# Kernel tuning notes

Measured on AMD Instinct MI355X. Metric: run time of the kernel, lower is better.

The kernel has to match this reference:

```python
import jax, jax.numpy as jnp
import numpy as np

N, H, DDE, NH = 256, 256, 64, 4

def setup_inputs() -> dict:
    key = jax.random.key(0)
    ks = jax.random.split(key, 12)
    rn = lambda k, s, sc=1.0: (jax.random.normal(k, s) * sc).astype(jnp.float32)
    return {
        "action_hidden_state": rn(ks[0], (N, H)),
        "goal_hidden_state": rn(ks[1], (N, H)),
        "goal": rn(ks[2], (N, 2)),
        "action": rn(ks[3], (N, 2)),
        "W_dist": rn(ks[4], (8, DDE), 0.3),          # distEmbedding Linear(8, dde)
        "b_dist": jnp.zeros((DDE,), jnp.float32),
        "W_gate": rn(ks[5], (DDE, H), 0.1),          # gateFC Linear(dde, H)
        "b_gate": jnp.zeros((H,), jnp.float32),
        "w": rn(ks[6], (NH, 1, H, H), 0.06),         # GAT per-head projection
        "a": rn(ks[7], (1, 1, 2 * H, 1), 0.06),      # attention vector
        "bias": jnp.zeros((H,), jnp.float32),
    }

def reference(action_hidden_state, goal_hidden_state, goal, action,
              W_dist, b_dist, W_gate, b_gate, w, a, bias):
    n = goal.shape[0]
    # --- InteractionGate.cal_gate: x1[i,j] = x[j], x2[i,j] = x[i] ---
    g1 = jnp.broadcast_to(goal[None, :, :], (n, n, 2))
    g2 = jnp.broadcast_to(goal[:, None, :], (n, n, 2))
    a1 = jnp.broadcast_to(action[None, :, :], (n, n, 2))
    a2 = jnp.broadcast_to(action[:, None, :], (n, n, 2))
    dist = jnp.concatenate([a2, g2, a1, g1], axis=-1)                 # [n,n,8]
    gate = jax.nn.sigmoid(jax.nn.relu(dist @ W_dist + b_dist) @ W_gate + b_gate)  # [n,n,H]
    # temp_action_1[i,j] = action_hidden_state[j]
    gate_action = gate * jnp.tanh(action_hidden_state[None, :, :])    # [n,n,H]
    # diagonal entries replaced by goal_hidden_state (mask_goal = eye)
    eye = jnp.eye(n, dtype=bool)[:, :, None]
    gated_h = jnp.where(eye, goal_hidden_state[None, :, :], gate_action)  # [n,n,H]

    # --- GAT assembly: h_self[i,k] = ahs[i]; h_other = cat(ahs, gated_h) ---
    h_other = jnp.concatenate([action_hidden_state[:, None, :], gated_h], axis=1)  # [n,n+1,H]

    wm = w[:, 0]          # [NH,H,H]
    a_flat = a[0, 0, :, 0]  # [2H]
    f = wm.shape[-1]
    n_head = wm.shape[0]
    # h_self rows along k are all identical -> project once per (head, node)
    hsp = jnp.einsum('nh,zhf->znf', action_hidden_state, wm)          # [NH,n,f]
    hop = jnp.einsum('nkh,zhf->znkf', h_other, wm)                    # [NH,n,n+1,f]
    # cat([h_self', h_other']) @ a  ==  h_self'@a[:f] + h_other'@a[f:]
    score = (hsp @ a_flat[:f])[:, :, None] + hop @ a_flat[f:]         # [NH,n,n+1]
    e = jnp.where(score > 0, score, 0.2 * score)                      # LeakyReLU(0.2)
    alpha = jax.nn.softmax(e, axis=-1)                                # softmax over neighbors
    # h_attn = matmul(h_other, w) == hop; weighted sum over k, mean over heads
    out = jnp.einsum('znk,znkf->nf', alpha, hop) / n_head             # [n,f]
    return jax.nn.relu(out) + bias
```

## Files before the change

kernel.cpp:

```cpp
#include <hip/hip_runtime.h>
#include <hip/hip_bf16.h>

#define NN 256
#define HH 256

typedef __attribute__((ext_vector_type(8))) short short8;
typedef __attribute__((ext_vector_type(4))) float f32x4;

__device__ __forceinline__ ushort f2bf(float x) {
    __hip_bfloat16 h = __float2bfloat16(x);
    return *reinterpret_cast<ushort*>(&h);
}
__device__ __forceinline__ float bf2f(ushort u) {
    __hip_bfloat16 h = *reinterpret_cast<__hip_bfloat16*>(&u);
    return __bfloat162float(h);
}
__device__ __forceinline__ float fast_rcp(float x) {
    return __builtin_amdgcn_rcpf(x);
}
__device__ __forceinline__ float fast_tanh(float x) {
    float e = __expf(2.0f * x);
    return 1.0f - 2.0f * fast_rcp(e + 1.0f);
}
template <int CTRL>
__device__ __forceinline__ float dpp_add(float x) {
    int y = __builtin_amdgcn_update_dpp(0, __float_as_int(x), CTRL, 0xF, 0xF, true);
    return x + __int_as_float(y);
}
template <int CTRL>
__device__ __forceinline__ float dpp_max(float x) {
    int y = __builtin_amdgcn_update_dpp(0, __float_as_int(x), CTRL, 0xF, 0xF, true);
    return fmaxf(x, __int_as_float(y));
}
__device__ __forceinline__ float red16(float v) {
    v = dpp_add<0xB1>(v); v = dpp_add<0x4E>(v);
    v = dpp_add<0x141>(v); v = dpp_add<0x140>(v);
    return v;
}
__device__ __forceinline__ float red16max(float v) {
    v = dpp_max<0xB1>(v); v = dpp_max<0x4E>(v);
    v = dpp_max<0x141>(v); v = dpp_max<0x140>(v);
    return v;
}

#define WS_P   0
#define WS_Q   16384
#define WS_T   32768
#define WS_WA  98304
#define WS_WB  99328
#define WS_WGT 100352
#define WS_PV  108544
#define WS_ML  632832
#define WS_W2H 636928
#define WS_W2L 768000

__global__ __launch_bounds__(256) void precompute_kernel(
    const float* __restrict__ ahs, const float* __restrict__ goal,
    const float* __restrict__ action, const float* __restrict__ Wd,
    const float* __restrict__ b_dist, const float* __restrict__ Wg,
    const float* __restrict__ w, const float* __restrict__ a,
    float* __restrict__ ws)
{
    const int b = blockIdx.x;
    const int t = threadIdx.x;
    const int wid  = t >> 6;
    const int lane = t & 63;
    float* P  = ws + WS_P;
    float* Q  = ws + WS_Q;
    float* T  = ws + WS_T;
    float* WA = ws + WS_WA;
    float* WB = ws + WS_WB;
    ushort* WgT  = (ushort*)(ws + WS_WGT);
    ushort* W2hi = (ushort*)(ws + WS_W2H);
    ushort* W2lo = (ushort*)(ws + WS_W2L);

    __shared__ __align__(16) float tile[64][65];

    if (b < 16) {
        const int z  = b >> 2;
        const int rg = b & 3;
        const int hbase = rg*64 + wid*16;
        const f32x4 aB = *(const f32x4*)(a + lane*4);
        const f32x4 aA = *(const f32x4*)(a + HH + lane*4);
#pragma unroll 4
        for (int rr = 0; rr < 16; ++rr) {
            const int h = hbase + rr;
            const f32x4 w4 = *(const f32x4*)(w + z*HH*HH + h*HH + lane*4);
            float dA = w4.x*aA.x + w4.y*aA.y + w4.z*aA.z + w4.w*aA.w;
            float dB = w4.x*aB.x + w4.y*aB.y + w4.z*aB.z + w4.w*aB.w;
#pragma unroll
            for (int off = 32; off; off >>= 1) {
                dA += __shfl_xor(dA, off);
                dB += __shfl_xor(dB, off);
            }
            if (lane == 0) { WA[z*HH + h] = dA; WB[z*HH + h] = dB; }
        }
    } else if (b < 80) {
        const int idx = b - 16;
        const int k0  = (idx >> 2) * 64;
        const int f0  = (idx & 3) * 64;
        const int ff  = t & 63;
#pragma unroll 4
        for (int i = 0; i < 16; ++i) {
            const int kk = i*4 + wid;
            tile[kk][ff] = w[(k0 + kk)*HH + f0 + ff];
        }
        __syncthreads();
#pragma unroll 4
        for (int i = 0; i < 16; ++i) {
            const int fl = i*4 + wid;
            float x = tile[ff][fl];
            ushort hi = f2bf(x);
            ushort lo = f2bf(x - bf2f(hi));
            W2hi[(size_t)(f0 + fl)*1024 + k0 + ff] = hi;
            W2lo[(size_t)(f0 + fl)*1024 + k0 + ff] = lo;
        }
    } else if (b < 144) {
        const int i = (b - 80)*4 + wid;
        const int d = lane;
        float a0 = action[2*i], a1 = action[2*i+1];
        float g0 = goal[2*i],   g1 = goal[2*i+1];
        P[i*64 + d] = a0*Wd[0*64+d] + a1*Wd[1*64+d]
                    + g0*Wd[2*64+d] + g1*Wd[3*64+d] + b_dist[d];
        Q[i*64 + d] = a0*Wd[4*64+d] + a1*Wd[5*64+d]
                    + g0*Wd[6*64+d] + g1*Wd[7*64+d];
    } else if (b < 208) {
        const int d = b - 144;
        WgT[t*64 + d] = f2bf(Wg[d*HH + t]);
    } else {
        const int idx = ((b - 208)*256 + t)*4;
        float4 v = *(const float4*)(ahs + idx);
        float4 o;
        o.x = fast_tanh(v.x); o.y = fast_tanh(v.y);
        o.z = fast_tanh(v.z); o.w = fast_tanh(v.w);
        *(float4*)(T + idx) = o;
    }
}

__global__ __launch_bounds__(256, 2) void gat_partial_kernel(
    const float* __restrict__ ahs, const float* __restrict__ ghs,
    const float* __restrict__ b_gate, float* __restrict__ ws)
{
    const int n    = blockIdx.x >> 1;
    const int hh   = blockIdx.x & 1;
    const int t    = threadIdx.x;
    const int wid  = t >> 6;
    const int lane = t & 63;
    const int quad = lane >> 4;
    const int l15  = lane & 15;
    const int zg   = quad;
    const int jj   = l15;
    const int n0   = wid * 64;

    const float* P  = ws + WS_P;
    const float* Q  = ws + WS_Q;
    const float* T  = ws + WS_T;
    const float* WA = ws + WS_WA;
    const float* WB = ws + WS_WB;
    const ushort* WgT = (const ushort*)(ws + WS_WGT);
    float* PV = ws + WS_PV;
    float* ML = ws + WS_ML;

    __shared__ __align__(16) float part[2][4][16][4];
    __shared__ __align__(16) float alpha_w[4][16][4];
    __shared__ __align__(16) float vred[16][260];
    __shared__ __align__(16) ushort A_l[128*64];

    int hcol[4];
#pragma unroll
    for (int nt = 0; nt < 4; ++nt) hcol[nt] = n0 + nt*16 + l15;

    short8 bfrag[4][2];
    float  wa_reg[4][4];
    float  bgv[4], gval[4];
#pragma unroll
    for (int nt = 0; nt < 4; ++nt) {
#pragma unroll
        for (int kh = 0; kh < 2; ++kh)
            bfrag[nt][kh] = *(const short8*)(WgT + hcol[nt]*64 + kh*32 + quad*8);
#pragma unroll
        for (int z = 0; z < 4; ++z) wa_reg[z][nt] = WA[z*HH + hcol[nt]];
        bgv[nt]  = b_gate[hcol[nt]];
        gval[nt] = ghs[n*HH + hcol[nt]];
    }

    {
        const int jl = t >> 1;
        const int kh = t & 1;
        const float* prow = P + n*64 + kh*32;
        const float* qrow = Q + (hh*128 + jl)*64 + kh*32;
        ushort hv[32];
#pragma unroll
        for (int c = 0; c < 8; ++c) {
            f32x4 pq = *(const f32x4*)(prow + c*4);
            f32x4 qq = *(const f32x4*)(qrow + c*4);
            hv[c*4+0] = f2bf(fmaxf(pq.x + qq.x, 0.f));
            hv[c*4+1] = f2bf(fmaxf(pq.y + qq.y, 0.f));
            hv[c*4+2] = f2bf(fmaxf(pq.z + qq.z, 0.f));
            hv[c*4+3] = f2bf(fmaxf(pq.w + qq.w, 0.f));
        }
        char* rb = (char*)A_l + jl*128;
        const int sw = (jl & 7) << 4;
#pragma unroll
        for (int c2 = 0; c2 < 4; ++c2) {
            const int off = (kh*64 + c2*16) ^ sw;
            *(short8*)(rb + off) = *(const short8*)(hv + c2*8);
        }
    }

    float vacc[4][4];
    {
        float av[4];
#pragma unroll
        for (int nt = 0; nt < 4; ++nt) av[nt] = ahs[n*HH + hcol[nt]];
#pragma unroll
        for (int z = 0; z < 4; ++z)
#pragma unroll
            for (int nt = 0; nt < 4; ++nt)
                vacc[z][nt] = (hh == 0 && quad == 0) ? av[nt] : 0.f;
    }

    float cz_r, m_r, l_r;
    {
        float pc = 0.f, ps = 0.f;
        const int hb = jj*16;
#pragma unroll
        for (int i4 = 0; i4 < 4; ++i4) {
            f32x4 av = *(const f32x4*)(ahs + n*HH + hb + i4*4);
            f32x4 wb = *(const f32x4*)(WB + zg*HH + hb + i4*4);
            f32x4 wa = *(const f32x4*)(WA + zg*HH + hb + i4*4);
            pc = fmaf(av.x, wb.x, pc); pc = fmaf(av.y, wb.y, pc);
            pc = fmaf(av.z, wb.z, pc); pc = fmaf(av.w, wb.w, pc);
            ps = fmaf(av.x, wa.x, ps); ps = fmaf(av.y, wa.y, ps);
            ps = fmaf(av.z, wa.z, ps); ps = fmaf(av.w, wa.w, ps);
        }
        pc = red16(pc); ps = red16(ps);
        cz_r = pc;
        if (hh == 0) {
            float sc = pc + ps;
            m_r = sc > 0.f ? sc : 0.2f * sc;
            l_r = 1.0f;
        } else {
            m_r = -__builtin_inff();
            l_r = 0.0f;
        }
    }

    __syncthreads();

    float tval[4][4];
    {
        const int j0 = hh*128;
#pragma unroll
        for (int r = 0; r < 4; ++r) {
            const int jg = j0 + quad*4 + r;
#pragma unroll
            for (int nt = 0; nt < 4; ++nt)
                tval[nt][r] = T[jg*HH + hcol[nt]];
        }
    }

    for (int cc = 0; cc < 8; ++cc) {
        const int j0  = hh*128 + cc*16;
        const int par = cc & 1;

        const int jl = cc*16 + l15;
        const char* rb = (const char*)A_l + jl*128;
        const int sw = (l15 & 7) << 4;
        short8 afrag0 = *(const short8*)(rb + ((quad*16) ^ sw));
        short8 afrag1 = *(const short8*)(rb + ((64 + quad*16) ^ sw));

        f32x4 acc[4];
#pragma unroll
        for (int nt = 0; nt < 4; ++nt) {
            f32x4 a4 = (f32x4){0.f,0.f,0.f,0.f};
            a4 = __builtin_amdgcn_mfma_f32_16x16x32_bf16(afrag0, bfrag[nt][0], a4, 0, 0, 0);
            a4 = __builtin_amdgcn_mfma_f32_16x16x32_bf16(afrag1, bfrag[nt][1], a4, 0, 0, 0);
            acc[nt] = a4;
        }

        float vals[4][4];
#pragma unroll
        for (int r = 0; r < 4; ++r) {
            const int jg = j0 + quad*4 + r;
            const bool diag = (jg == n);
#pragma unroll
            for (int nt = 0; nt < 4; ++nt) {
                float u = acc[nt][r] + bgv[nt];
                float g = fast_rcp(1.0f + __expf(-u));
                vals[nt][r] = diag ? gval[nt] : g * tval[nt][r];
            }
        }

#pragma unroll
        for (int z = 0; z < 4; ++z) {
            float pp[4];
#pragma unroll
            for (int r = 0; r < 4; ++r) {
                float s = 0.f;
#pragma unroll
                for (int nt = 0; nt < 4; ++nt)
                    s = fmaf(vals[nt][r], wa_reg[z][nt], s);
                pp[r] = red16(s);
            }
            if (l15 == z) {
#pragma unroll
                for (int r = 0; r < 4; ++r)
                    part[par][z][quad*4 + r][wid] = pp[r];
            }
        }
        __syncthreads();

        float tnext[4][4];
        if (cc < 7) {
            const int j1 = j0 + 16;
#pragma unroll
            for (int r = 0; r < 4; ++r) {
                const int jg = j1 + quad*4 + r;
#pragma unroll
                for (int nt = 0; nt < 4; ++nt)
                    tnext[nt][r] = T[jg*HH + hcol[nt]];
            }
        }

        float scl0, scl1, scl2, scl3;
        {
            f32x4 pr = *(const f32x4*)&part[par][zg][jj][0];
            float s = cz_r + ((pr.x + pr.y) + (pr.z + pr.w));
            float e = s > 0.f ? s : 0.2f * s;
            float mx = red16max(e);
            float m_new = fmaxf(m_r, mx);
            float at = __expf(e - m_new);
            float ss = red16(at);
            float scale = __expf(m_r - m_new);
            l_r = l_r * scale + ss;
            m_r = m_new;
            alpha_w[wid][jj][zg] = at;
            scl0 = __shfl(scale, 0);
            scl1 = __shfl(scale, 16);
            scl2 = __shfl(scale, 32);
            scl3 = __shfl(scale, 48);
        }
#pragma unroll
        for (int nt = 0; nt < 4; ++nt) {
            vacc[0][nt] *= scl0; vacc[1][nt] *= scl1;
            vacc[2][nt] *= scl2; vacc[3][nt] *= scl3;
        }
#pragma unroll
        for (int r = 0; r < 4; ++r) {
            f32x4 al = *(const f32x4*)&alpha_w[wid][quad*4 + r][0];
#pragma unroll
            for (int nt = 0; nt < 4; ++nt) {
                float v = vals[nt][r];
                vacc[0][nt] = fmaf(al.x, v, vacc[0][nt]);
                vacc[1][nt] = fmaf(al.y, v, vacc[1][nt]);
                vacc[2][nt] = fmaf(al.z, v, vacc[2][nt]);
                vacc[3][nt] = fmaf(al.w, v, vacc[3][nt]);
            }
        }
        if (cc < 7) {
#pragma unroll
            for (int nt = 0; nt < 4; ++nt)
#pragma unroll
                for (int r = 0; r < 4; ++r)
                    tval[nt][r] = tnext[nt][r];
        }
    }

#pragma unroll
    for (int z = 0; z < 4; ++z)
#pragma unroll
        for (int nt = 0; nt < 4; ++nt)
            vred[quad*4 + z][hcol[nt]] = vacc[z][nt];
    __syncthreads();
#pragma unroll
    for (int z = 0; z < 4; ++z) {
        float s = (vred[0*4+z][t] + vred[1*4+z][t]) + (vred[2*4+z][t] + vred[3*4+z][t]);
        PV[((size_t)(hh*4 + z)*NN + n)*HH + t] = s;
    }
    if (wid == 0 && l15 == 0) {
        ML[((hh*4 + zg)*NN + n)*2 + 0] = m_r;
        ML[((hh*4 + zg)*NN + n)*2 + 1] = l_r;
    }
}

__global__ __launch_bounds__(256) void gat_out_kernel(
    const float* __restrict__ bias, const float* __restrict__ ws,
    float* __restrict__ out)
{
    const int n0 = (blockIdx.x >> 4) * 16;
    const int f0 = (blockIdx.x & 15) * 16;
    const int t    = threadIdx.x;
    const int wid  = t >> 6;
    const int lane = t & 63;
    const int quad = lane >> 4;
    const int l15  = lane & 15;

    const float* PV = ws + WS_PV;
    const float* ML = ws + WS_ML;
    const ushort* W2hi = (const ushort*)(ws + WS_W2H);
    const ushort* W2lo = (const ushort*)(ws + WS_W2L);

    __shared__ __align__(16) float redc[3][16][17];
    __shared__ __align__(16) float sq[16][4][2];

    if (t < 128) {
        const int n_i = t >> 3, z = (t >> 1) & 3, q = t & 1;
        float m = ML[((q*4 + z)*NN + n0 + n_i)*2 + 0];
        float l = ML[((q*4 + z)*NN + n0 + n_i)*2 + 1];
        float mm = fmaxf(m, __shfl_xor(m, 1));
        float s  = __expf(m - mm);
        float ls = l * s;
        ls += __shfl_xor(ls, 1);
        sq[n_i][z][q] = s * fast_rcp(ls);
    }
    __syncthreads();

    f32x4 acc = (f32x4){0.f,0.f,0.f,0.f};

    const float s0 = sq[l15][wid][0];
    const float s1 = sq[l15][wid][1];
    const float* pv0 = PV + ((size_t)(0*4 + wid)*NN + n0 + l15)*HH;
    const float* pv1 = PV + ((size_t)(1*4 + wid)*NN + n0 + l15)*HH;

    for (int ks = 0; ks < 8; ++ks) {
        const int kp = ks*32 + quad*8;
        f32x4 p0a = *(const f32x4*)(pv0 + kp);
        f32x4 p0b = *(const f32x4*)(pv0 + kp + 4);
        f32x4 p1a = *(const f32x4*)(pv1 + kp);
        f32x4 p1b = *(const f32x4*)(pv1 + kp + 4);
        float v[8];
        v[0] = s0*p0a.x + s1*p1a.x; v[1] = s0*p0a.y + s1*p1a.y;
        v[2] = s0*p0a.z + s1*p1a.z; v[3] = s0*p0a.w + s1*p1a.w;
        v[4] = s0*p0b.x + s1*p1b.x; v[5] = s0*p0b.y + s1*p1b.y;
        v[6] = s0*p0b.z + s1*p1b.z; v[7] = s0*p0b.w + s1*p1b.w;
        ushort hi[8], lo[8];
#pragma unroll
        for (int c = 0; c < 8; ++c) {
            hi[c] = f2bf(v[c]);
            lo[c] = f2bf(v[c] - bf2f(hi[c]));
        }
        short8 ah = *(short8*)hi;
        short8 al = *(short8*)lo;
        const size_t boff = (size_t)(f0 + l15)*1024 + wid*256 + kp;
        short8 bh = *(const short8*)(W2hi + boff);
        short8 bl = *(const short8*)(W2lo + boff);
        acc = __builtin_amdgcn_mfma_f32_16x16x32_bf16(ah, bh, acc, 0, 0, 0);
        acc = __builtin_amdgcn_mfma_f32_16x16x32_bf16(ah, bl, acc, 0, 0, 0);
        acc = __builtin_amdgcn_mfma_f32_16x16x32_bf16(al, bh, acc, 0, 0, 0);
    }

    if (wid > 0) {
#pragma unroll
        for (int r = 0; r < 4; ++r)
            redc[wid-1][quad*4 + r][l15] = acc[r];
    }
    __syncthreads();
    if (wid == 0) {
        const int f = f0 + l15;
        float bv = bias[f];
#pragma unroll
        for (int r = 0; r < 4; ++r) {
            const int row = quad*4 + r;
            float s = acc[r]
                    + redc[0][row][l15]
                    + redc[1][row][l15]
                    + redc[2][row][l15];
            out[(size_t)(n0 + row)*HH + f] = fmaxf(0.25f * s, 0.f) + bv;
        }
    }
}

extern "C" void kernel_launch(void* const* d_in, const int* in_sizes, int n_in,
                              void* d_out, int out_size, void* d_ws, size_t ws_size,
                              hipStream_t stream)
{
    const float* ahs    = (const float*)d_in[0];
    const float* ghs    = (const float*)d_in[1];
    const float* goal   = (const float*)d_in[2];
    const float* action = (const float*)d_in[3];
    const float* Wd     = (const float*)d_in[4];
    const float* b_dist = (const float*)d_in[5];
    const float* Wg     = (const float*)d_in[6];
    const float* b_gate = (const float*)d_in[7];
    const float* w      = (const float*)d_in[8];
    const float* a      = (const float*)d_in[9];
    const float* bias   = (const float*)d_in[10];
    float* ws   = (float*)d_ws;
    float* outp = (float*)d_out;

    precompute_kernel<<<272, 256, 0, stream>>>(ahs, goal, action, Wd, b_dist, Wg, w, a, ws);
    gat_partial_kernel<<<512, 256, 0, stream>>>(ahs, ghs, b_gate, ws);
    gat_out_kernel<<<256, 256, 0, stream>>>(bias, ws, outp);
}
```

Baseline: 114.6 us.

## Fuse three kernels into one cooperative kernel with grid-wide syncs

Merges the precompute, GAT partial and output kernels into a single cooperative launch of 512 blocks, with grid.sync between phases and a union of shared-memory layouts. The goal is to remove two kernel launch gaps and the tail drain between dependent kernels. In exchange it adds the cost of grid-wide barriers, and it requires all 512 blocks to be resident at once. It falls back to the three-kernel path if the cooperative launch fails.

```diff
diff --git a/kernel.cpp b/kernel.cpp
--- a/kernel.cpp
+++ b/kernel.cpp
@@ -1,5 +1,8 @@
 #include <hip/hip_runtime.h>
 #include <hip/hip_bf16.h>
+#include <hip/hip_cooperative_groups.h>
+
+namespace cg = cooperative_groups;
 
 #define NN 256
 #define HH 256
@@ -53,6 +56,421 @@
 #define WS_ML  632832
 #define WS_W2H 636928
 #define WS_W2L 768000
+
+__global__ __launch_bounds__(256, 2) void fused_kernel(
+    const float* __restrict__ ahs, const float* __restrict__ ghs,
+    const float* __restrict__ goal, const float* __restrict__ action,
+    const float* __restrict__ Wd, const float* __restrict__ b_dist,
+    const float* __restrict__ Wg, const float* __restrict__ b_gate,
+    const float* __restrict__ w, const float* __restrict__ a,
+    const float* __restrict__ bias,
+    float* __restrict__ ws, float* __restrict__ out)
+{
+    cg::grid_group gridg = cg::this_grid();
+
+    __shared__ __align__(16) union {
+        struct { float tile[64][65]; } pa;
+        struct {
+            float part[2][4][16][4];
+            float alpha_w[4][16][4];
+            float vred[16][260];
+            ushort A_l[128*64];
+        } pb;
+        struct { float redc[3][16][17]; float sq[16][4][2]; } pc;
+    } sm;
+
+    float* P  = ws + WS_P;
+    float* Q  = ws + WS_Q;
+    float* T  = ws + WS_T;
+    float* WA = ws + WS_WA;
+    float* WB = ws + WS_WB;
+    ushort* WgT  = (ushort*)(ws + WS_WGT);
+    ushort* W2hi = (ushort*)(ws + WS_W2H);
+    ushort* W2lo = (ushort*)(ws + WS_W2L);
+    float* PV = ws + WS_PV;
+    float* ML = ws + WS_ML;
+
+    {
+        const int b = blockIdx.x;
+        const int t = threadIdx.x;
+        const int wid  = t >> 6;
+        const int lane = t & 63;
+
+        if (b < 16) {
+            const int z  = b >> 2;
+            const int rg = b & 3;
+            const int hbase = rg*64 + wid*16;
+            const f32x4 aB = *(const f32x4*)(a + lane*4);
+            const f32x4 aA = *(const f32x4*)(a + HH + lane*4);
+#pragma unroll 4
+            for (int rr = 0; rr < 16; ++rr) {
+                const int h = hbase + rr;
+                const f32x4 w4 = *(const f32x4*)(w + z*HH*HH + h*HH + lane*4);
+                float dA = w4.x*aA.x + w4.y*aA.y + w4.z*aA.z + w4.w*aA.w;
+                float dB = w4.x*aB.x + w4.y*aB.y + w4.z*aB.z + w4.w*aB.w;
+#pragma unroll
+                for (int off = 32; off; off >>= 1) {
+                    dA += __shfl_xor(dA, off);
+                    dB += __shfl_xor(dB, off);
+                }
+                if (lane == 0) { WA[z*HH + h] = dA; WB[z*HH + h] = dB; }
+            }
+        } else if (b < 80) {
+            const int idx = b - 16;
+            const int k0  = (idx >> 2) * 64;
+            const int f0  = (idx & 3) * 64;
+            const int ff  = t & 63;
+#pragma unroll 4
+            for (int i = 0; i < 16; ++i) {
+                const int kk = i*4 + wid;
+                sm.pa.tile[kk][ff] = w[(k0 + kk)*HH + f0 + ff];
+            }
+            __syncthreads();
+#pragma unroll 4
+            for (int i = 0; i < 16; ++i) {
+                const int fl = i*4 + wid;
+                float x = sm.pa.tile[ff][fl];
+                ushort hi = f2bf(x);
+                ushort lo = f2bf(x - bf2f(hi));
+                W2hi[(size_t)(f0 + fl)*1024 + k0 + ff] = hi;
+                W2lo[(size_t)(f0 + fl)*1024 + k0 + ff] = lo;
+            }
+        } else if (b < 144) {
+            const int i = (b - 80)*4 + wid;
+            const int d = lane;
+            float a0 = action[2*i], a1 = action[2*i+1];
+            float g0 = goal[2*i],   g1 = goal[2*i+1];
+            P[i*64 + d] = a0*Wd[0*64+d] + a1*Wd[1*64+d]
+                        + g0*Wd[2*64+d] + g1*Wd[3*64+d] + b_dist[d];
+            Q[i*64 + d] = a0*Wd[4*64+d] + a1*Wd[5*64+d]
+                        + g0*Wd[6*64+d] + g1*Wd[7*64+d];
+        } else if (b < 208) {
+            const int d = b - 144;
+            WgT[t*64 + d] = f2bf(Wg[d*HH + t]);
+        } else if (b < 272) {
+            const int idx = ((b - 208)*256 + t)*4;
+            float4 v = *(const float4*)(ahs + idx);
+            float4 o;
+            o.x = fast_tanh(v.x); o.y = fast_tanh(v.y);
+            o.z = fast_tanh(v.z); o.w = fast_tanh(v.w);
+            *(float4*)(T + idx) = o;
+        }
+    }
+
+    __threadfence();
+    gridg.sync();
+
+    {
+        const int n    = blockIdx.x >> 1;
+        const int hh   = blockIdx.x & 1;
+        const int t    = threadIdx.x;
+        const int wid  = t >> 6;
+        const int lane = t & 63;
+        const int quad = lane >> 4;
+        const int l15  = lane & 15;
+        const int zg   = quad;
+        const int jj   = l15;
+        const int n0   = wid * 64;
+
+        int hcol[4];
+#pragma unroll
+        for (int nt = 0; nt < 4; ++nt) hcol[nt] = n0 + nt*16 + l15;
+
+        short8 bfrag[4][2];
+        float  wa_reg[4][4];
+        float  bgv[4], gval[4];
+#pragma unroll
+        for (int nt = 0; nt < 4; ++nt) {
+#pragma unroll
+            for (int kh = 0; kh < 2; ++kh)
+                bfrag[nt][kh] = *(const short8*)(WgT + hcol[nt]*64 + kh*32 + quad*8);
+#pragma unroll
+            for (int z = 0; z < 4; ++z) wa_reg[z][nt] = WA[z*HH + hcol[nt]];
+            bgv[nt]  = b_gate[hcol[nt]];
+            gval[nt] = ghs[n*HH + hcol[nt]];
+        }
+
+        {
+            const int jl = t >> 1;
+            const int kh = t & 1;
+            const float* prow = P + n*64 + kh*32;
+            const float* qrow = Q + (hh*128 + jl)*64 + kh*32;
+            ushort hv[32];
+#pragma unroll
+            for (int c = 0; c < 8; ++c) {
+                f32x4 pq = *(const f32x4*)(prow + c*4);
+                f32x4 qq = *(const f32x4*)(qrow + c*4);
+                hv[c*4+0] = f2bf(fmaxf(pq.x + qq.x, 0.f));
+                hv[c*4+1] = f2bf(fmaxf(pq.y + qq.y, 0.f));
+                hv[c*4+2] = f2bf(fmaxf(pq.z + qq.z, 0.f));
+                hv[c*4+3] = f2bf(fmaxf(pq.w + qq.w, 0.f));
+            }
+            char* rb = (char*)sm.pb.A_l + jl*128;
+            const int sw = (jl & 7) << 4;
+#pragma unroll
+            for (int c2 = 0; c2 < 4; ++c2) {
+                const int off = (kh*64 + c2*16) ^ sw;
+                *(short8*)(rb + off) = *(const short8*)(hv + c2*8);
+            }
+        }
+
+        float vacc[4][4];
+        {
+            float av[4];
+#pragma unroll
+            for (int nt = 0; nt < 4; ++nt) av[nt] = ahs[n*HH + hcol[nt]];
+#pragma unroll
+            for (int z = 0; z < 4; ++z)
+#pragma unroll
+                for (int nt = 0; nt < 4; ++nt)
+                    vacc[z][nt] = (hh == 0 && quad == 0) ? av[nt] : 0.f;
+        }
+
+        float cz_r, m_r, l_r;
+        {
+            float pc = 0.f, ps = 0.f;
+            const int hb = jj*16;
+#pragma unroll
+            for (int i4 = 0; i4 < 4; ++i4) {
+                f32x4 av = *(const f32x4*)(ahs + n*HH + hb + i4*4);
+                f32x4 wb = *(const f32x4*)(WB + zg*HH + hb + i4*4);
+                f32x4 wa = *(const f32x4*)(WA + zg*HH + hb + i4*4);
+                pc = fmaf(av.x, wb.x, pc); pc = fmaf(av.y, wb.y, pc);
+                pc = fmaf(av.z, wb.z, pc); pc = fmaf(av.w, wb.w, pc);
+                ps = fmaf(av.x, wa.x, ps); ps = fmaf(av.y, wa.y, ps);
+                ps = fmaf(av.z, wa.z, ps); ps = fmaf(av.w, wa.w, ps);
+            }
+            pc = red16(pc); ps = red16(ps);
+            cz_r = pc;
+            if (hh == 0) {
+                float sc = pc + ps;
+                m_r = sc > 0.f ? sc : 0.2f * sc;
+                l_r = 1.0f;
+            } else {
+                m_r = -__builtin_inff();
+                l_r = 0.0f;
+            }
+        }
+
+        __syncthreads();
+
+        float tval[4][4];
+        {
+            const int j0 = hh*128;
+#pragma unroll
+            for (int r = 0; r < 4; ++r) {
+                const int jg = j0 + quad*4 + r;
+#pragma unroll
+                for (int nt = 0; nt < 4; ++nt)
+                    tval[nt][r] = T[jg*HH + hcol[nt]];
+            }
+        }
+
+        for (int cc = 0; cc < 8; ++cc) {
+            const int j0  = hh*128 + cc*16;
+            const int par = cc & 1;
+
+            const int jl = cc*16 + l15;
+            const char* rb = (const char*)sm.pb.A_l + jl*128;
+            const int sw = (l15 & 7) << 4;
+            short8 afrag0 = *(const short8*)(rb + ((quad*16) ^ sw));
+            short8 afrag1 = *(const short8*)(rb + ((64 + quad*16) ^ sw));
+
+            f32x4 acc[4];
+#pragma unroll
+            for (int nt = 0; nt < 4; ++nt) {
+                f32x4 a4 = (f32x4){0.f,0.f,0.f,0.f};
+                a4 = __builtin_amdgcn_mfma_f32_16x16x32_bf16(afrag0, bfrag[nt][0], a4, 0, 0, 0);
+                a4 = __builtin_amdgcn_mfma_f32_16x16x32_bf16(afrag1, bfrag[nt][1], a4, 0, 0, 0);
+                acc[nt] = a4;
+            }
+
+            float vals[4][4];
+#pragma unroll
+            for (int r = 0; r < 4; ++r) {
+                const int jg = j0 + quad*4 + r;
+                const bool diag = (jg == n);
+#pragma unroll
+                for (int nt = 0; nt < 4; ++nt) {
+                    float u = acc[nt][r] + bgv[nt];
+                    float g = fast_rcp(1.0f + __expf(-u));
+                    vals[nt][r] = diag ? gval[nt] : g * tval[nt][r];
+                }
+            }
+
+#pragma unroll
+            for (int z = 0; z < 4; ++z) {
+                float pp[4];
+#pragma unroll
+                for (int r = 0; r < 4; ++r) {
+                    float s = 0.f;
+#pragma unroll
+                    for (int nt = 0; nt < 4; ++nt)
+                        s = fmaf(vals[nt][r], wa_reg[z][nt], s);
+                    pp[r] = red16(s);
+                }
+                if (l15 == z) {
+#pragma unroll
+                    for (int r = 0; r < 4; ++r)
+                        sm.pb.part[par][z][quad*4 + r][wid] = pp[r];
+                }
+            }
+            __syncthreads();
+
+            float tnext[4][4];
+            if (cc < 7) {
+                const int j1 = j0 + 16;
+#pragma unroll
+                for (int r = 0; r < 4; ++r) {
+                    const int jg = j1 + quad*4 + r;
+#pragma unroll
+                    for (int nt = 0; nt < 4; ++nt)
+                        tnext[nt][r] = T[jg*HH + hcol[nt]];
+                }
+            }
+
+            float scl0, scl1, scl2, scl3;
+            {
+                f32x4 pr = *(const f32x4*)&sm.pb.part[par][zg][jj][0];
+                float s = cz_r + ((pr.x + pr.y) + (pr.z + pr.w));
+                float e = s > 0.f ? s : 0.2f * s;
+                float mx = red16max(e);
+                float m_new = fmaxf(m_r, mx);
+                float at = __expf(e - m_new);
+                float ss = red16(at);
+                float scale = __expf(m_r - m_new);
+                l_r = l_r * scale + ss;
+                m_r = m_new;
+                sm.pb.alpha_w[wid][jj][zg] = at;
+                scl0 = __shfl(scale, 0);
+                scl1 = __shfl(scale, 16);
+                scl2 = __shfl(scale, 32);
+                scl3 = __shfl(scale, 48);
+            }
+#pragma unroll
+            for (int nt = 0; nt < 4; ++nt) {
+                vacc[0][nt] *= scl0; vacc[1][nt] *= scl1;
+                vacc[2][nt] *= scl2; vacc[3][nt] *= scl3;
+            }
+#pragma unroll
+            for (int r = 0; r < 4; ++r) {
+                f32x4 al = *(const f32x4*)&sm.pb.alpha_w[wid][quad*4 + r][0];
+#pragma unroll
+                for (int nt = 0; nt < 4; ++nt) {
+                    float v = vals[nt][r];
+                    vacc[0][nt] = fmaf(al.x, v, vacc[0][nt]);
+                    vacc[1][nt] = fmaf(al.y, v, vacc[1][nt]);
+                    vacc[2][nt] = fmaf(al.z, v, vacc[2][nt]);
+                    vacc[3][nt] = fmaf(al.w, v, vacc[3][nt]);
+                }
+            }
+            if (cc < 7) {
+#pragma unroll
+                for (int nt = 0; nt < 4; ++nt)
+#pragma unroll
+                    for (int r = 0; r < 4; ++r)
+                        tval[nt][r] = tnext[nt][r];
+            }
+        }
+
+#pragma unroll
+        for (int z = 0; z < 4; ++z)
+#pragma unroll
+            for (int nt = 0; nt < 4; ++nt)
+                sm.pb.vred[quad*4 + z][hcol[nt]] = vacc[z][nt];
+        __syncthreads();
+#pragma unroll
+        for (int z = 0; z < 4; ++z) {
+            float s = (sm.pb.vred[0*4+z][t] + sm.pb.vred[1*4+z][t])
+                    + (sm.pb.vred[2*4+z][t] + sm.pb.vred[3*4+z][t]);
+            PV[((size_t)(hh*4 + z)*NN + n)*HH + t] = s;
+        }
+        if (wid == 0 && l15 == 0) {
+            ML[((hh*4 + zg)*NN + n)*2 + 0] = m_r;
+            ML[((hh*4 + zg)*NN + n)*2 + 1] = l_r;
+        }
+    }
+
+    __threadfence();
+    gridg.sync();
+
+    if (blockIdx.x < 256) {
+        const int b = blockIdx.x;
+        const int n0 = (b >> 4) * 16;
+        const int f0 = (b & 15) * 16;
+        const int t    = threadIdx.x;
+        const int wid  = t >> 6;
+        const int lane = t & 63;
+        const int quad = lane >> 4;
+        const int l15  = lane & 15;
+
+        if (t < 128) {
+            const int n_i = t >> 3, z = (t >> 1) & 3, q = t & 1;
+            float m = ML[((q*4 + z)*NN + n0 + n_i)*2 + 0];
+            float l = ML[((q*4 + z)*NN + n0 + n_i)*2 + 1];
+            float mm = fmaxf(m, __shfl_xor(m, 1));
+            float s  = __expf(m - mm);
+            float ls = l * s;
+            ls += __shfl_xor(ls, 1);
+            sm.pc.sq[n_i][z][q] = s * fast_rcp(ls);
+        }
+        __syncthreads();
+
+        f32x4 acc = (f32x4){0.f,0.f,0.f,0.f};
+
+        const float s0 = sm.pc.sq[l15][wid][0];
+        const float s1 = sm.pc.sq[l15][wid][1];
+        const float* pv0 = PV + ((size_t)(0*4 + wid)*NN + n0 + l15)*HH;
+        const float* pv1 = PV + ((size_t)(1*4 + wid)*NN + n0 + l15)*HH;
+
+        for (int ks = 0; ks < 8; ++ks) {
+            const int kp = ks*32 + quad*8;
+            f32x4 p0a = *(const f32x4*)(pv0 + kp);
+            f32x4 p0b = *(const f32x4*)(pv0 + kp + 4);
+            f32x4 p1a = *(const f32x4*)(pv1 + kp);
+            f32x4 p1b = *(const f32x4*)(pv1 + kp + 4);
+            float v[8];
+            v[0] = s0*p0a.x + s1*p1a.x; v[1] = s0*p0a.y + s1*p1a.y;
+            v[2] = s0*p0a.z + s1*p1a.z; v[3] = s0*p0a.w + s1*p1a.w;
+            v[4] = s0*p0b.x + s1*p1b.x; v[5] = s0*p0b.y + s1*p1b.y;
+            v[6] = s0*p0b.z + s1*p1b.z; v[7] = s0*p0b.w + s1*p1b.w;
+            ushort hi[8], lo[8];
+#pragma unroll
+            for (int c = 0; c < 8; ++c) {
+                hi[c] = f2bf(v[c]);
+                lo[c] = f2bf(v[c] - bf2f(hi[c]));
+            }
+            short8 ah = *(short8*)hi;
+            short8 al = *(short8*)lo;
+            const size_t boff = (size_t)(f0 + l15)*1024 + wid*256 + kp;
+            short8 bh = *(const short8*)(W2hi + boff);
+            short8 bl = *(const short8*)(W2lo + boff);
+            acc = __builtin_amdgcn_mfma_f32_16x16x32_bf16(ah, bh, acc, 0, 0, 0);
+            acc = __builtin_amdgcn_mfma_f32_16x16x32_bf16(ah, bl, acc, 0, 0, 0);
+            acc = __builtin_amdgcn_mfma_f32_16x16x32_bf16(al, bh, acc, 0, 0, 0);
+        }
+
+        if (wid > 0) {
+#pragma unroll
+            for (int r = 0; r < 4; ++r)
+                sm.pc.redc[wid-1][quad*4 + r][l15] = acc[r];
+        }
+        __syncthreads();
+        if (wid == 0) {
+            const int f = f0 + l15;
+            float bv = bias[f];
+#pragma unroll
+            for (int r = 0; r < 4; ++r) {
+                const int row = quad*4 + r;
+                float s = acc[r]
+                        + sm.pc.redc[0][row][l15]
+                        + sm.pc.redc[1][row][l15]
+                        + sm.pc.redc[2][row][l15];
+                out[(size_t)(n0 + row)*HH + f] = fmaxf(0.25f * s, 0.f) + bv;
+            }
+        }
+    }
+}
 
 __global__ __launch_bounds__(256) void precompute_kernel(
     const float* __restrict__ ahs, const float* __restrict__ goal,
@@ -489,7 +907,16 @@
     float* ws   = (float*)d_ws;
     float* outp = (float*)d_out;
 
-    precompute_kernel<<<272, 256, 0, stream>>>(ahs, goal, action, Wd, b_dist, Wg, w, a, ws);
-    gat_partial_kernel<<<512, 256, 0, stream>>>(ahs, ghs, b_gate, ws);
-    gat_out_kernel<<<256, 256, 0, stream>>>(bias, ws, outp);
-}
+    void* args[] = {
+        (void*)&ahs, (void*)&ghs, (void*)&goal, (void*)&action,
+        (void*)&Wd, (void*)&b_dist, (void*)&Wg, (void*)&b_gate,
+        (void*)&w, (void*)&a, (void*)&bias, (void*)&ws, (void*)&outp
+    };
+    hipError_t err = hipLaunchCooperativeKernel(
+        (void*)fused_kernel, dim3(512), dim3(256), args, 0, stream);
+    if (err != hipSuccess) {
+        precompute_kernel<<<272, 256, 0, stream>>>(ahs, goal, action, Wd, b_dist, Wg, w, a, ws);
+        gat_partial_kernel<<<512, 256, 0, stream>>>(ahs, ghs, b_gate, ws);
+        gat_out_kernel<<<256, 256, 0, stream>>>(bias, ws, outp);
+    }
+}
```

Result: slower. 333.1 us (+190.7%).

## Fuse GAT partial and output kernels using per-tile atomic counters

Applied to the files above, without the earlier changes.

Merges the partial-attention kernel and the output kernel into one launch. Each block bumps a per-16-node counter after writing its PV/ML partials. The hh==0 blocks then spin until all 32 contributing blocks of their tile have arrived, and compute the output tile for that tile. This removes one kernel launch and its boundary, and shares shared memory through a union. The spin-wait relies on all contributing blocks being co-resident or scheduled ahead, which risks stalls, and a guard counter breaks out of the spin.

```diff
diff --git a/kernel.cpp b/kernel.cpp
--- a/kernel.cpp
+++ b/kernel.cpp
@@ -53,6 +53,8 @@
 #define WS_ML  632832
 #define WS_W2H 636928
 #define WS_W2L 768000
+
+__device__ unsigned int g_cnt[16];
 
 __global__ __launch_bounds__(256) void precompute_kernel(
     const float* __restrict__ ahs, const float* __restrict__ goal,
@@ -76,6 +78,9 @@
 
     __shared__ __align__(16) float tile[64][65];
 
+    if (b == 0 && t < 16)
+        __hip_atomic_store(&g_cnt[t], 0u, __ATOMIC_RELAXED, __HIP_MEMORY_SCOPE_AGENT);
+
     if (b < 16) {
         const int z  = b >> 2;
         const int rg = b & 3;
@@ -137,9 +142,10 @@
     }
 }
 
-__global__ __launch_bounds__(256, 2) void gat_partial_kernel(
+__global__ __launch_bounds__(256, 2) void gat_partial_out_kernel(
     const float* __restrict__ ahs, const float* __restrict__ ghs,
-    const float* __restrict__ b_gate, float* __restrict__ ws)
+    const float* __restrict__ b_gate, const float* __restrict__ bias,
+    float* __restrict__ ws, float* __restrict__ out)
 {
     const int n    = blockIdx.x >> 1;
     const int hh   = blockIdx.x & 1;
@@ -161,253 +167,270 @@
     float* PV = ws + WS_PV;
     float* ML = ws + WS_ML;
 
-    __shared__ __align__(16) float part[2][4][16][4];
-    __shared__ __align__(16) float alpha_w[4][16][4];
-    __shared__ __align__(16) float vred[16][260];
-    __shared__ __align__(16) ushort A_l[128*64];
-
-    int hcol[4];
-#pragma unroll
-    for (int nt = 0; nt < 4; ++nt) hcol[nt] = n0 + nt*16 + l15;
-
-    short8 bfrag[4][2];
-    float  wa_reg[4][4];
-    float  bgv[4], gval[4];
-#pragma unroll
-    for (int nt = 0; nt < 4; ++nt) {
-#pragma unroll
-        for (int kh = 0; kh < 2; ++kh)
-            bfrag[nt][kh] = *(const short8*)(WgT + hcol[nt]*64 + kh*32 + quad*8);
-#pragma unroll
-        for (int z = 0; z < 4; ++z) wa_reg[z][nt] = WA[z*HH + hcol[nt]];
-        bgv[nt]  = b_gate[hcol[nt]];
-        gval[nt] = ghs[n*HH + hcol[nt]];
-    }
+    __shared__ __align__(16) union {
+        struct {
+            float part[2][4][16][4];
+            float alpha_w[4][16][4];
+            float vred[16][260];
+            ushort A_l[128*64];
+        } pb;
+        struct { float redc[3][16][17]; float sq[16][4][2]; } pc;
+    } sm;
 
     {
-        const int jl = t >> 1;
-        const int kh = t & 1;
-        const float* prow = P + n*64 + kh*32;
-        const float* qrow = Q + (hh*128 + jl)*64 + kh*32;
-        ushort hv[32];
-#pragma unroll
-        for (int c = 0; c < 8; ++c) {
-            f32x4 pq = *(const f32x4*)(prow + c*4);
-            f32x4 qq = *(const f32x4*)(qrow + c*4);
-            hv[c*4+0] = f2bf(fmaxf(pq.x + qq.x, 0.f));
-            hv[c*4+1] = f2bf(fmaxf(pq.y + qq.y, 0.f));
-            hv[c*4+2] = f2bf(fmaxf(pq.z + qq.z, 0.f));
-            hv[c*4+3] = f2bf(fmaxf(pq.w + qq.w, 0.f));
-        }
-        char* rb = (char*)A_l + jl*128;
-        const int sw = (jl & 7) << 4;
-#pragma unroll
-        for (int c2 = 0; c2 < 4; ++c2) {
-            const int off = (kh*64 + c2*16) ^ sw;
-            *(short8*)(rb + off) = *(const short8*)(hv + c2*8);
-        }
-    }
-
-    float vacc[4][4];
-    {
-        float av[4];
-#pragma unroll
-        for (int nt = 0; nt < 4; ++nt) av[nt] = ahs[n*HH + hcol[nt]];
+        auto& part    = sm.pb.part;
+        auto& alpha_w = sm.pb.alpha_w;
+        auto& vred    = sm.pb.vred;
+        auto& A_l     = sm.pb.A_l;
+
+        int hcol[4];
+#pragma unroll
+        for (int nt = 0; nt < 4; ++nt) hcol[nt] = n0 + nt*16 + l15;
+
+        short8 bfrag[4][2];
+        float  wa_reg[4][4];
+        float  bgv[4], gval[4];
+#pragma unroll
+        for (int nt = 0; nt < 4; ++nt) {
+#pragma unroll
+            for (int kh = 0; kh < 2; ++kh)
+                bfrag[nt][kh] = *(const short8*)(WgT + hcol[nt]*64 + kh*32 + quad*8);
+#pragma unroll
+            for (int z = 0; z < 4; ++z) wa_reg[z][nt] = WA[z*HH + hcol[nt]];
+            bgv[nt]  = b_gate[hcol[nt]];
+            gval[nt] = ghs[n*HH + hcol[nt]];
+        }
+
+        {
+            const int jl = t >> 1;
+            const int kh = t & 1;
+            const float* prow = P + n*64 + kh*32;
+            const float* qrow = Q + (hh*128 + jl)*64 + kh*32;
+            ushort hv[32];
+#pragma unroll
+            for (int c = 0; c < 8; ++c) {
+                f32x4 pq = *(const f32x4*)(prow + c*4);
+                f32x4 qq = *(const f32x4*)(qrow + c*4);
+                hv[c*4+0] = f2bf(fmaxf(pq.x + qq.x, 0.f));
+                hv[c*4+1] = f2bf(fmaxf(pq.y + qq.y, 0.f));
+                hv[c*4+2] = f2bf(fmaxf(pq.z + qq.z, 0.f));
+                hv[c*4+3] = f2bf(fmaxf(pq.w + qq.w, 0.f));
+            }
+            char* rb = (char*)A_l + jl*128;
+            const int sw = (jl & 7) << 4;
+#pragma unroll
+            for (int c2 = 0; c2 < 4; ++c2) {
+                const int off = (kh*64 + c2*16) ^ sw;
+                *(short8*)(rb + off) = *(const short8*)(hv + c2*8);
+            }
+        }
+
+        float vacc[4][4];
+        {
+            float av[4];
+#pragma unroll
+            for (int nt = 0; nt < 4; ++nt) av[nt] = ahs[n*HH + hcol[nt]];
+#pragma unroll
+            for (int z = 0; z < 4; ++z)
+#pragma unroll
+                for (int nt = 0; nt < 4; ++nt)
+                    vacc[z][nt] = (hh == 0 && quad == 0) ? av[nt] : 0.f;
+        }
+
+        float cz_r, m_r, l_r;
+        {
+            float pc = 0.f, ps = 0.f;
+            const int hb = jj*16;
+#pragma unroll
+            for (int i4 = 0; i4 < 4; ++i4) {
+                f32x4 av = *(const f32x4*)(ahs + n*HH + hb + i4*4);
+                f32x4 wb = *(const f32x4*)(WB + zg*HH + hb + i4*4);
+                f32x4 wa = *(const f32x4*)(WA + zg*HH + hb + i4*4);
+                pc = fmaf(av.x, wb.x, pc); pc = fmaf(av.y, wb.y, pc);
+                pc = fmaf(av.z, wb.z, pc); pc = fmaf(av.w, wb.w, pc);
+                ps = fmaf(av.x, wa.x, ps); ps = fmaf(av.y, wa.y, ps);
+                ps = fmaf(av.z, wa.z, ps); ps = fmaf(av.w, wa.w, ps);
+            }
+            pc = red16(pc); ps = red16(ps);
+            cz_r = pc;
+            if (hh == 0) {
+                float sc = pc + ps;
+                m_r = sc > 0.f ? sc : 0.2f * sc;
+                l_r = 1.0f;
+            } else {
+                m_r = -__builtin_inff();
+                l_r = 0.0f;
+            }
+        }
+
+        __syncthreads();
+
+        float tval[4][4];
+        {
+            const int j0 = hh*128;
+#pragma unroll
+            for (int r = 0; r < 4; ++r) {
+                const int jg = j0 + quad*4 + r;
+#pragma unroll
+                for (int nt = 0; nt < 4; ++nt)
+                    tval[nt][r] = T[jg*HH + hcol[nt]];
+            }
+        }
+
+        for (int cc = 0; cc < 8; ++cc) {
+            const int j0  = hh*128 + cc*16;
+            const int par = cc & 1;
+
+            const int jl = cc*16 + l15;
+            const char* rb = (const char*)A_l + jl*128;
+            const int sw = (l15 & 7) << 4;
+            short8 afrag0 = *(const short8*)(rb + ((quad*16) ^ sw));
+            short8 afrag1 = *(const short8*)(rb + ((64 + quad*16) ^ sw));
+
+            f32x4 acc[4];
+#pragma unroll
+            for (int nt = 0; nt < 4; ++nt) {
+                f32x4 a4 = (f32x4){0.f,0.f,0.f,0.f};
+                a4 = __builtin_amdgcn_mfma_f32_16x16x32_bf16(afrag0, bfrag[nt][0], a4, 0, 0, 0);
+                a4 = __builtin_amdgcn_mfma_f32_16x16x32_bf16(afrag1, bfrag[nt][1], a4, 0, 0, 0);
+                acc[nt] = a4;
+            }
+
+            float vals[4][4];
+#pragma unroll
+            for (int r = 0; r < 4; ++r) {
+                const int jg = j0 + quad*4 + r;
+                const bool diag = (jg == n);
+#pragma unroll
+                for (int nt = 0; nt < 4; ++nt) {
+                    float u = acc[nt][r] + bgv[nt];
+                    float g = fast_rcp(1.0f + __expf(-u));
+                    vals[nt][r] = diag ? gval[nt] : g * tval[nt][r];
+                }
+            }
+
+#pragma unroll
+            for (int z = 0; z < 4; ++z) {
+                float pp[4];
+#pragma unroll
+                for (int r = 0; r < 4; ++r) {
+                    float s = 0.f;
+#pragma unroll
+                    for (int nt = 0; nt < 4; ++nt)
+                        s = fmaf(vals[nt][r], wa_reg[z][nt], s);
+                    pp[r] = red16(s);
+                }
+                if (l15 == z) {
+#pragma unroll
+                    for (int r = 0; r < 4; ++r)
+                        part[par][z][quad*4 + r][wid] = pp[r];
+                }
+            }
+            __syncthreads();
+
+            float tnext[4][4];
+            if (cc < 7) {
+                const int j1 = j0 + 16;
+#pragma unroll
+                for (int r = 0; r < 4; ++r) {
+                    const int jg = j1 + quad*4 + r;
+#pragma unroll
+                    for (int nt = 0; nt < 4; ++nt)
+                        tnext[nt][r] = T[jg*HH + hcol[nt]];
+                }
+            }
+
+            float scl0, scl1, scl2, scl3;
+            {
+                f32x4 pr = *(const f32x4*)&part[par][zg][jj][0];
+                float s = cz_r + ((pr.x + pr.y) + (pr.z + pr.w));
+                float e = s > 0.f ? s : 0.2f * s;
+                float mx = red16max(e);
+                float m_new = fmaxf(m_r, mx);
+                float at = __expf(e - m_new);
+                float ss = red16(at);
+                float scale = __expf(m_r - m_new);
+                l_r = l_r * scale + ss;
+                m_r = m_new;
+                alpha_w[wid][jj][zg] = at;
+                scl0 = __shfl(scale, 0);
+                scl1 = __shfl(scale, 16);
+                scl2 = __shfl(scale, 32);
+                scl3 = __shfl(scale, 48);
+            }
+#pragma unroll
+            for (int nt = 0; nt < 4; ++nt) {
+                vacc[0][nt] *= scl0; vacc[1][nt] *= scl1;
+                vacc[2][nt] *= scl2; vacc[3][nt] *= scl3;
+            }
+#pragma unroll
+            for (int r = 0; r < 4; ++r) {
+                f32x4 al = *(const f32x4*)&alpha_w[wid][quad*4 + r][0];
+#pragma unroll
+                for (int nt = 0; nt < 4; ++nt) {
+                    float v = vals[nt][r];
+                    vacc[0][nt] = fmaf(al.x, v, vacc[0][nt]);
+                    vacc[1][nt] = fmaf(al.y, v, vacc[1][nt]);
+                    vacc[2][nt] = fmaf(al.z, v, vacc[2][nt]);
+                    vacc[3][nt] = fmaf(al.w, v, vacc[3][nt]);
+                }
+            }
+            if (cc < 7) {
+#pragma unroll
+                for (int nt = 0; nt < 4; ++nt)
+#pragma unroll
+                    for (int r = 0; r < 4; ++r)
+                        tval[nt][r] = tnext[nt][r];
+            }
+        }
+
 #pragma unroll
         for (int z = 0; z < 4; ++z)
 #pragma unroll
             for (int nt = 0; nt < 4; ++nt)
-                vacc[z][nt] = (hh == 0 && quad == 0) ? av[nt] : 0.f;
-    }
-
-    float cz_r, m_r, l_r;
-    {
-        float pc = 0.f, ps = 0.f;
-        const int hb = jj*16;
-#pragma unroll
-        for (int i4 = 0; i4 < 4; ++i4) {
-            f32x4 av = *(const f32x4*)(ahs + n*HH + hb + i4*4);
-            f32x4 wb = *(const f32x4*)(WB + zg*HH + hb + i4*4);
-            f32x4 wa = *(const f32x4*)(WA + zg*HH + hb + i4*4);
-            pc = fmaf(av.x, wb.x, pc); pc = fmaf(av.y, wb.y, pc);
-            pc = fmaf(av.z, wb.z, pc); pc = fmaf(av.w, wb.w, pc);
-            ps = fmaf(av.x, wa.x, ps); ps = fmaf(av.y, wa.y, ps);
-            ps = fmaf(av.z, wa.z, ps); ps = fmaf(av.w, wa.w, ps);
-        }
-        pc = red16(pc); ps = red16(ps);
-        cz_r = pc;
-        if (hh == 0) {
-            float sc = pc + ps;
-            m_r = sc > 0.f ? sc : 0.2f * sc;
-            l_r = 1.0f;
-        } else {
-            m_r = -__builtin_inff();
-            l_r = 0.0f;
-        }
-    }
-
+                vred[quad*4 + z][hcol[nt]] = vacc[z][nt];
+        __syncthreads();
+#pragma unroll
+        for (int z = 0; z < 4; ++z) {
+            float s = (vred[0*4+z][t] + vred[1*4+z][t]) + (vred[2*4+z][t] + vred[3*4+z][t]);
+            PV[((size_t)(hh*4 + z)*NN + n)*HH + t] = s;
+        }
+        if (wid == 0 && l15 == 0) {
+            ML[((hh*4 + zg)*NN + n)*2 + 0] = m_r;
+            ML[((hh*4 + zg)*NN + n)*2 + 1] = l_r;
+        }
+    }
+
+    __threadfence();
     __syncthreads();
-
-    float tval[4][4];
-    {
-        const int j0 = hh*128;
-#pragma unroll
-        for (int r = 0; r < 4; ++r) {
-            const int jg = j0 + quad*4 + r;
-#pragma unroll
-            for (int nt = 0; nt < 4; ++nt)
-                tval[nt][r] = T[jg*HH + hcol[nt]];
-        }
-    }
-
-    for (int cc = 0; cc < 8; ++cc) {
-        const int j0  = hh*128 + cc*16;
-        const int par = cc & 1;
-
-        const int jl = cc*16 + l15;
-        const char* rb = (const char*)A_l + jl*128;
-        const int sw = (l15 & 7) << 4;
-        short8 afrag0 = *(const short8*)(rb + ((quad*16) ^ sw));
-        short8 afrag1 = *(const short8*)(rb + ((64 + quad*16) ^ sw));
-
-        f32x4 acc[4];
-#pragma unroll
-        for (int nt = 0; nt < 4; ++nt) {
-            f32x4 a4 = (f32x4){0.f,0.f,0.f,0.f};
-            a4 = __builtin_amdgcn_mfma_f32_16x16x32_bf16(afrag0, bfrag[nt][0], a4, 0, 0, 0);
-            a4 = __builtin_amdgcn_mfma_f32_16x16x32_bf16(afrag1, bfrag[nt][1], a4, 0, 0, 0);
-            acc[nt] = a4;
-        }
-
-        float vals[4][4];
-#pragma unroll
-        for (int r = 0; r < 4; ++r) {
-            const int jg = j0 + quad*4 + r;
-            const bool diag = (jg == n);
-#pragma unroll
-            for (int nt = 0; nt < 4; ++nt) {
-                float u = acc[nt][r] + bgv[nt];
-                float g = fast_rcp(1.0f + __expf(-u));
-                vals[nt][r] = diag ? gval[nt] : g * tval[nt][r];
-            }
-        }
-
-#pragma unroll
-        for (int z = 0; z < 4; ++z) {
-            float pp[4];
-#pragma unroll
-            for (int r = 0; r < 4; ++r) {
-                float s = 0.f;
-#pragma unroll
-                for (int nt = 0; nt < 4; ++nt)
-                    s = fmaf(vals[nt][r], wa_reg[z][nt], s);
-                pp[r] = red16(s);
-            }
-            if (l15 == z) {
-#pragma unroll
-                for (int r = 0; r < 4; ++r)
-                    part[par][z][quad*4 + r][wid] = pp[r];
-            }
-        }
-        __syncthreads();
-
-        float tnext[4][4];
-        if (cc < 7) {
-            const int j1 = j0 + 16;
-#pragma unroll
-            for (int r = 0; r < 4; ++r) {
-                const int jg = j1 + quad*4 + r;
-#pragma unroll
-                for (int nt = 0; nt < 4; ++nt)
-                    tnext[nt][r] = T[jg*HH + hcol[nt]];
-            }
-        }
-
-        float scl0, scl1, scl2, scl3;
-        {
-            f32x4 pr = *(const f32x4*)&part[par][zg][jj][0];
-            float s = cz_r + ((pr.x + pr.y) + (pr.z + pr.w));
-            float e = s > 0.f ? s : 0.2f * s;
-            float mx = red16max(e);
-            float m_new = fmaxf(m_r, mx);
-            float at = __expf(e - m_new);
-            float ss = red16(at);
-            float scale = __expf(m_r - m_new);
-            l_r = l_r * scale + ss;
-            m_r = m_new;
-            alpha_w[wid][jj][zg] = at;
-            scl0 = __shfl(scale, 0);
-            scl1 = __shfl(scale, 16);
-            scl2 = __shfl(scale, 32);
-            scl3 = __shfl(scale, 48);
-        }
-#pragma unroll
-        for (int nt = 0; nt < 4; ++nt) {
-            vacc[0][nt] *= scl0; vacc[1][nt] *= scl1;
-            vacc[2][nt] *= scl2; vacc[3][nt] *= scl3;
-        }
-#pragma unroll
-        for (int r = 0; r < 4; ++r) {
-            f32x4 al = *(const f32x4*)&alpha_w[wid][quad*4 + r][0];
-#pragma unroll
-            for (int nt = 0; nt < 4; ++nt) {
-                float v = vals[nt][r];
-                vacc[0][nt] = fmaf(al.x, v, vacc[0][nt]);
-                vacc[1][nt] = fmaf(al.y, v, vacc[1][nt]);
-                vacc[2][nt] = fmaf(al.z, v, vacc[2][nt]);
-                vacc[3][nt] = fmaf(al.w, v, vacc[3][nt]);
-            }
-        }
-        if (cc < 7) {
-#pragma unroll
-            for (int nt = 0; nt < 4; ++nt)
-#pragma unroll
-                for (int r = 0; r < 4; ++r)
-                    tval[nt][r] = tnext[nt][r];
-        }
-    }
-
-#pragma unroll
-    for (int z = 0; z < 4; ++z)
-#pragma unroll
-        for (int nt = 0; nt < 4; ++nt)
-            vred[quad*4 + z][hcol[nt]] = vacc[z][nt];
+    if (t == 0)
+        __hip_atomic_fetch_add(&g_cnt[n >> 4], 1u, __ATOMIC_RELEASE, __HIP_MEMORY_SCOPE_AGENT);
+
+    if (hh != 0) return;
+
+    const int ti = n >> 4;
+    const int n0o = ti * 16;
+    const int f0 = (n & 15) * 16;
+
+    if (t == 0) {
+        unsigned int guard = 0;
+        while (__hip_atomic_load(&g_cnt[ti], __ATOMIC_ACQUIRE, __HIP_MEMORY_SCOPE_AGENT) < 32u) {
+            __builtin_amdgcn_s_sleep(1);
+            if (++guard > 0x20000000u) break;
+        }
+    }
     __syncthreads();
-#pragma unroll
-    for (int z = 0; z < 4; ++z) {
-        float s = (vred[0*4+z][t] + vred[1*4+z][t]) + (vred[2*4+z][t] + vred[3*4+z][t]);
-        PV[((size_t)(hh*4 + z)*NN + n)*HH + t] = s;
-    }
-    if (wid == 0 && l15 == 0) {
-        ML[((hh*4 + zg)*NN + n)*2 + 0] = m_r;
-        ML[((hh*4 + zg)*NN + n)*2 + 1] = l_r;
-    }
-}
-
-__global__ __launch_bounds__(256) void gat_out_kernel(
-    const float* __restrict__ bias, const float* __restrict__ ws,
-    float* __restrict__ out)
-{
-    const int n0 = (blockIdx.x >> 4) * 16;
-    const int f0 = (blockIdx.x & 15) * 16;
-    const int t    = threadIdx.x;
-    const int wid  = t >> 6;
-    const int lane = t & 63;
-    const int quad = lane >> 4;
-    const int l15  = lane & 15;
-
-    const float* PV = ws + WS_PV;
-    const float* ML = ws + WS_ML;
+    (void)__hip_atomic_load(&g_cnt[ti], __ATOMIC_ACQUIRE, __HIP_MEMORY_SCOPE_AGENT);
+
+    auto& redc = sm.pc.redc;
+    auto& sq   = sm.pc.sq;
     const ushort* W2hi = (const ushort*)(ws + WS_W2H);
     const ushort* W2lo = (const ushort*)(ws + WS_W2L);
 
-    __shared__ __align__(16) float redc[3][16][17];
-    __shared__ __align__(16) float sq[16][4][2];
-
     if (t < 128) {
         const int n_i = t >> 3, z = (t >> 1) & 3, q = t & 1;
-        float m = ML[((q*4 + z)*NN + n0 + n_i)*2 + 0];
-        float l = ML[((q*4 + z)*NN + n0 + n_i)*2 + 1];
+        float m = ML[((q*4 + z)*NN + n0o + n_i)*2 + 0];
+        float l = ML[((q*4 + z)*NN + n0o + n_i)*2 + 1];
         float mm = fmaxf(m, __shfl_xor(m, 1));
         float s  = __expf(m - mm);
         float ls = l * s;
@@ -420,8 +443,8 @@
 
     const float s0 = sq[l15][wid][0];
     const float s1 = sq[l15][wid][1];
-    const float* pv0 = PV + ((size_t)(0*4 + wid)*NN + n0 + l15)*HH;
-    const float* pv1 = PV + ((size_t)(1*4 + wid)*NN + n0 + l15)*HH;
+    const float* pv0 = PV + ((size_t)(0*4 + wid)*NN + n0o + l15)*HH;
+    const float* pv1 = PV + ((size_t)(1*4 + wid)*NN + n0o + l15)*HH;
 
     for (int ks = 0; ks < 8; ++ks) {
         const int kp = ks*32 + quad*8;
@@ -466,7 +489,7 @@
                     + redc[0][row][l15]
                     + redc[1][row][l15]
                     + redc[2][row][l15];
-            out[(size_t)(n0 + row)*HH + f] = fmaxf(0.25f * s, 0.f) + bv;
+            out[(size_t)(n0o + row)*HH + f] = fmaxf(0.25f * s, 0.f) + bv;
         }
     }
 }
@@ -490,6 +513,5 @@
     float* outp = (float*)d_out;
 
     precompute_kernel<<<272, 256, 0, stream>>>(ahs, goal, action, Wd, b_dist, Wg, w, a, ws);
-    gat_partial_kernel<<<512, 256, 0, stream>>>(ahs, ghs, b_gate, ws);
-    gat_out_kernel<<<256, 256, 0, stream>>>(bias, ws, outp);
-}
+    gat_partial_out_kernel<<<512, 256, 0, stream>>>(ahs, ghs, b_gate, bias, ws, outp);
+}
```

After: 187.7 us. +63.7%, slower.
